# Kernel tuning notes

Measured on AMD Instinct MI355X. Metric: run time of the kernel, lower is better.

## Reference

```python
import jax, jax.numpy as jnp
import numpy as np

B, N, D = 8, 2048, 512
H, DH = 8, 64
SCALE = DH ** -0.5


def setup_inputs() -> dict:
    key = jax.random.key(0)
    ks = jax.random.split(key, 7)
    x = jax.random.normal(ks[0], (B, N, D), dtype=jnp.float32)
    mask = jax.random.uniform(ks[1], (B, N, N), dtype=jnp.float32)
    Wq = jax.random.normal(ks[2], (D, H * DH), dtype=jnp.float32) * (D ** -0.5)
    Wk = jax.random.normal(ks[3], (D, H * DH), dtype=jnp.float32) * (D ** -0.5)
    Wv = jax.random.normal(ks[4], (D, H * DH), dtype=jnp.float32) * (D ** -0.5)
    Wo = jax.random.normal(ks[5], (H * DH, D), dtype=jnp.float32) * ((H * DH) ** -0.5)
    bo = jnp.zeros((D,), dtype=jnp.float32)
    return {"x": x, "mask": mask, "Wq": Wq, "Wk": Wk, "Wv": Wv, "Wo": Wo, "bo": bo}


def reference(x, mask, Wq, Wk, Wv, Wo, bo):
    b, n, d = x.shape
    # QKV projections -> [b, h, n, dh]
    q = (x @ Wq).reshape(b, n, H, DH).transpose(0, 2, 1, 3)
    k = (x @ Wk).reshape(b, n, H, DH).transpose(0, 2, 1, 3)
    v = (x @ Wv).reshape(b, n, H, DH).transpose(0, 2, 1, 3)
    # scores with multiplicative structural mask bias: dots * (1 + M)
    dots = jnp.einsum('bhid,bhjd->bhij', q, k) * SCALE
    dots = dots * (1.0 + mask[:, None, :, :])
    attn = jax.nn.softmax(dots, axis=-1)  # dropout is identity in eval
    out = jnp.einsum('bhij,bhjd->bhid', attn, v)
    out = out.transpose(0, 2, 1, 3).reshape(b, n, H * DH)
    return out @ Wo + bo
```

## Files before the change

### kernel.cpp

```cpp
#include <hip/hip_runtime.h>

typedef __bf16 bf16;
typedef __bf16 bf16x8 __attribute__((ext_vector_type(8)));
typedef float  f32x4  __attribute__((ext_vector_type(4)));

#define B_  8
#define N_  2048
#define D_  512
#define H_  8
#define DH_ 64
static constexpr float SC2 = 0.18033688011112042f;

#if defined(__has_builtin)
#if __has_builtin(__builtin_amdgcn_exp2f)
#define EXP2(x) __builtin_amdgcn_exp2f(x)
#else
#define EXP2(x) exp2f(x)
#endif
#else
#define EXP2(x) exp2f(x)
#endif

__device__ __forceinline__ f32x4 mfma16(bf16x8 a, bf16x8 b, f32x4 c) {
  return __builtin_amdgcn_mfma_f32_16x16x32_bf16(a, b, c, 0, 0, 0);
}

__device__ __forceinline__ void gload_lds16(const void* g, void* l) {
  __builtin_amdgcn_global_load_lds((__attribute__((address_space(1))) void*)g,
                                   (__attribute__((address_space(3))) void*)l, 16, 0, 0);
}

__global__ void k_cvt_x(const float* __restrict__ x, bf16* __restrict__ xb) {
  int i = blockIdx.x * blockDim.x + threadIdx.x;
  const float4* p = (const float4*)x;
  float4 a = p[2*i], b = p[2*i+1];
  bf16x8 o;
  o[0]=(bf16)a.x; o[1]=(bf16)a.y; o[2]=(bf16)a.z; o[3]=(bf16)a.w;
  o[4]=(bf16)b.x; o[5]=(bf16)b.y; o[6]=(bf16)b.z; o[7]=(bf16)b.w;
  ((bf16x8*)xb)[i] = o;
}

__global__ void k_wt(const float* __restrict__ w, bf16* __restrict__ wt) {
  __shared__ float t[64][65];
  const int c0 = blockIdx.x * 64, k0 = blockIdx.y * 64;
  const int r = threadIdx.x >> 2, q4 = (threadIdx.x & 3) * 16;
#pragma unroll
  for (int j = 0; j < 16; j += 4) {
    float4 v = *(const float4*)(w + (k0 + r) * 512 + c0 + q4 + j);
    t[r][q4+j] = v.x; t[r][q4+j+1] = v.y; t[r][q4+j+2] = v.z; t[r][q4+j+3] = v.w;
  }
  __syncthreads();
  const int c = threadIdx.x >> 2, kq = (threadIdx.x & 3) * 16;
  bf16x8 o0, o1;
#pragma unroll
  for (int j = 0; j < 8; ++j) { o0[j] = (bf16)t[kq+j][c]; o1[j] = (bf16)t[kq+8+j][c]; }
  *(bf16x8*)(wt + (c0 + c) * 512 + k0 + kq) = o0;
  *(bf16x8*)(wt + (c0 + c) * 512 + k0 + kq + 8) = o1;
}

template<int MODE>
__global__ void k_gemm(const bf16* __restrict__ A, const bf16* __restrict__ Bt,
                       bf16* __restrict__ qo, bf16* __restrict__ ko, bf16* __restrict__ vo,
                       float* __restrict__ outp, const float* __restrict__ bo) {
  __shared__ bf16 lA[128 * 64];
  __shared__ bf16 lB[128 * 64];
  const int tid = threadIdx.x;
  const int wid = tid >> 6, lane = tid & 63;
  const int l15 = lane & 15, lq = lane >> 4;
  const int wr = wid >> 1, wc = wid & 1;
  const long long rowtile = (long long)blockIdx.x * 128;
  const long long coltile = (long long)blockIdx.y * 128;

  const bf16* gA[4]; const bf16* gB[4];
  bf16* lAc[4]; bf16* lBc[4];
#pragma unroll
  for (int i = 0; i < 4; ++i) {
    int ci = wid * 4 + i;
    int row = ci * 8 + (lane >> 3);
    int c8 = (lane & 7) ^ (row & 7);
    gA[i] = A + (rowtile + row) * 512 + c8 * 8;
    gB[i] = Bt + (coltile + row) * 512 + c8 * 8;
    lAc[i] = &lA[ci * 512];
    lBc[i] = &lB[ci * 512];
  }
  unsigned aoff[4][2], boff[4][2];
#pragma unroll
  for (int mi = 0; mi < 4; ++mi) {
#pragma unroll
    for (int ks = 0; ks < 2; ++ks) {
      int R = l15 + 16 * mi + 64 * wr;
      aoff[mi][ks] = R * 128 + ((((ks << 2) | lq) ^ (R & 7)) << 4);
      int Rb = l15 + 16 * mi + 64 * wc;
      boff[mi][ks] = Rb * 128 + ((((ks << 2) | lq) ^ (Rb & 7)) << 4);
    }
  }
  f32x4 acc[4][4] = {};
  for (int kt = 0; kt < 8; ++kt) {
#pragma unroll
    for (int i = 0; i < 4; ++i) gload_lds16(gA[i], lAc[i]);
#pragma unroll
    for (int i = 0; i < 4; ++i) gload_lds16(gB[i], lBc[i]);
#pragma unroll
    for (int i = 0; i < 4; ++i) { gA[i] += 64; gB[i] += 64; }
    __syncthreads();
#pragma unroll
    for (int ks = 0; ks < 2; ++ks) {
      bf16x8 af[4], bfr[4];
#pragma unroll
      for (int mi = 0; mi < 4; ++mi) af[mi] = *(const bf16x8*)((const char*)lA + aoff[mi][ks]);
#pragma unroll
      for (int nf = 0; nf < 4; ++nf) bfr[nf] = *(const bf16x8*)((const char*)lB + boff[nf][ks]);
#pragma unroll
      for (int mi = 0; mi < 4; ++mi)
#pragma unroll
        for (int nf = 0; nf < 4; ++nf)
          acc[mi][nf] = mfma16(af[mi], bfr[nf], acc[mi][nf]);
    }
    __syncthreads();
  }
  if (MODE == 0) {
#pragma unroll
    for (int nf = 0; nf < 4; ++nf) {
      const int col = (int)coltile + 64 * wc + nf * 16 + l15;
      const int mat = col >> 9, c5 = col & 511, hh = c5 >> 6, dh = c5 & 63;
#pragma unroll
      for (int mi = 0; mi < 4; ++mi) {
#pragma unroll
        for (int r = 0; r < 4; ++r) {
          const int R = (int)rowtile + 64 * wr + mi * 16 + lq * 4 + r;
          const int bb = R >> 11, n = R & 2047;
          const bf16 bv = (bf16)acc[mi][nf][r];
          const long long bh = bb * 8 + hh;
          if (mat == 0)      qo[(bh * 2048 + n) * 64 + dh] = bv;
          else if (mat == 1) ko[(bh * 2048 + n) * 64 + dh] = bv;
          else               vo[(bh * 64 + dh) * 2048 + n] = bv;
        }
      }
    }
  } else {
#pragma unroll
    for (int nf = 0; nf < 4; ++nf) {
      const int col = (int)coltile + 64 * wc + nf * 16 + l15;
      const float bias = bo[col];
#pragma unroll
      for (int mi = 0; mi < 4; ++mi)
#pragma unroll
        for (int r = 0; r < 4; ++r) {
          const long long R = rowtile + 64 * wr + mi * 16 + lq * 4 + r;
          outp[R * 512 + col] = acc[mi][nf][r] + bias;
        }
    }
  }
}

__global__ __launch_bounds__(512, 4) void k_attn(
    const bf16* __restrict__ qb, const bf16* __restrict__ kb, const bf16* __restrict__ vt,
    const float* __restrict__ mask, bf16* __restrict__ ao) {
  __shared__ bf16 kvb[2][2][64 * 64];
  __shared__ bf16 pb[8][16 * 64];
  const int tid = threadIdx.x;
  const int wid = tid >> 6, lane = tid & 63;
  const int l15 = lane & 15, lq = lane >> 4;
  const int p = blockIdx.x;
  const int xcd = p & 7, kk = p >> 3;
  const int g = xcd * 16 + (kk >> 3), h = kk & 7;
  const int b = g >> 4, qt = g & 15;
  const long long bh = b * 8 + h;
  const bf16* Q = qb + bh * (2048ll * 64);
  const bf16* K = kb + bh * (2048ll * 64);
  const bf16* V = vt + bh * (64ll * 2048);
  const int qrow0 = qt * 128 + wid * 16;
  const float* mbase = mask + ((long long)b * 2048 + qrow0 + lq * 4) * 2048 + l15;

  const int srow = tid >> 3;
  const int sc = (tid & 7) ^ (srow & 7);
  const bf16* kg = K + srow * 64 + sc * 8;
  const bf16* vg = V + srow * 2048 + sc * 8;
  bf16* kl0 = &kvb[0][0][tid * 8]; bf16* vl0 = &kvb[0][1][tid * 8];
  bf16* kl1 = &kvb[1][0][tid * 8]; bf16* vl1 = &kvb[1][1][tid * 8];
  char* pw = (char*)&pb[wid][0];

  bf16x8 qf[2];
#pragma unroll
  for (int ks = 0; ks < 2; ++ks)
    qf[ks] = *(const bf16x8*)(Q + (qrow0 + l15) * 64 + ks * 32 + lq * 8);

  f32x4 o[4] = {};
  float lsum[4] = {};
  float mA[16], mB[16];

  auto mload = [&](float (&m)[16], int jb) {
#pragma unroll
    for (int nf = 0; nf < 4; ++nf)
#pragma unroll
      for (int r = 0; r < 4; ++r)
        m[nf * 4 + r] = mbase[r * 2048 + jb + nf * 16];
  };

  auto compute = [&](int bi, const float (&m)[16]) {
    const bf16* kbL = &kvb[bi][0][0];
    const bf16* vbL = &kvb[bi][1][0];
    f32x4 s[4];
#pragma unroll
    for (int nf = 0; nf < 4; ++nf) {
      const int row = nf * 16 + l15;
      const bf16x8 kf = *(const bf16x8*)(kbL + row * 64 + ((lq ^ (row & 7)) << 3));
      f32x4 z = {0.f, 0.f, 0.f, 0.f};
      s[nf] = mfma16(qf[0], kf, z);
    }
#pragma unroll
    for (int nf = 0; nf < 4; ++nf) {
      const int row = nf * 16 + l15;
      const bf16x8 kf = *(const bf16x8*)(kbL + row * 64 + (((4 + lq) ^ (row & 7)) << 3));
      s[nf] = mfma16(qf[1], kf, s[nf]);
    }
#pragma unroll
    for (int nf = 0; nf < 4; ++nf) {
#pragma unroll
      for (int r = 0; r < 4; ++r) {
        const float dsc = s[nf][r] * SC2;
        const float pe = EXP2(fmaf(dsc, m[nf * 4 + r], dsc));
        lsum[r] += pe;
        const int colL = nf * 16 + l15;
        const int slot = ((colL >> 3) ^ (lq << 1) ^ r) & 7;
        *(bf16*)(pw + (lq * 4 + r) * 128 + slot * 16 + ((colL & 7) << 1)) = (bf16)pe;
      }
    }
#pragma unroll
    for (int ks = 0; ks < 2; ++ks) {
      const int c = ks * 4 + lq;
      const int slotp = (c ^ ((l15 >> 2) << 1) ^ (l15 & 3)) & 7;
      const bf16x8 pa = *(const bf16x8*)(pw + l15 * 128 + slotp * 16);
#pragma unroll
      for (int nf = 0; nf < 4; ++nf) {
        const int row = nf * 16 + l15;
        const bf16x8 vf = *(const bf16x8*)(vbL + row * 64 + ((c ^ (row & 7)) << 3));
        o[nf] = mfma16(pa, vf, o[nf]);
      }
    }
  };

  gload_lds16(kg, kl0); gload_lds16(vg, vl0);
  mload(mA, 0);
  __syncthreads();

  for (int jt = 0; jt < 32; jt += 2) {
    gload_lds16(kg + (jt + 1) * 4096, kl1);
    gload_lds16(vg + (jt + 1) * 64, vl1);
    mload(mB, (jt + 1) * 64);
    compute(0, mA);
    __syncthreads();
    if (jt + 2 < 32) {
      gload_lds16(kg + (jt + 2) * 4096, kl0);
      gload_lds16(vg + (jt + 2) * 64, vl0);
      mload(mA, (jt + 2) * 64);
    }
    compute(1, mB);
    __syncthreads();
  }

  float rinv[4];
#pragma unroll
  for (int r = 0; r < 4; ++r) {
    float v2 = lsum[r];
    v2 += __shfl_xor(v2, 1); v2 += __shfl_xor(v2, 2);
    v2 += __shfl_xor(v2, 4); v2 += __shfl_xor(v2, 8);
    rinv[r] = 1.0f / v2;
  }
#pragma unroll
  for (int nf = 0; nf < 4; ++nf)
#pragma unroll
    for (int r = 0; r < 4; ++r) {
      const long long rowg = (long long)b * 2048 + qrow0 + lq * 4 + r;
      ao[rowg * 512 + h * 64 + nf * 16 + l15] = (bf16)(o[nf][r] * rinv[r]);
    }
}

extern "C" void kernel_launch(void* const* d_in, const int* in_sizes, int n_in,
                              void* d_out, int out_size, void* d_ws, size_t ws_size,
                              hipStream_t stream) {
  const float* x    = (const float*)d_in[0];
  const float* mask = (const float*)d_in[1];
  const float* Wq   = (const float*)d_in[2];
  const float* Wk   = (const float*)d_in[3];
  const float* Wv   = (const float*)d_in[4];
  const float* Wo   = (const float*)d_in[5];
  const float* bo   = (const float*)d_in[6];
  float* out = (float*)d_out;
  char* ws = (char*)d_ws;

  const size_t SZ_XB = (size_t)16384 * 512 * 2;
  const size_t SZ_W3 = (size_t)1536 * 512 * 2;
  const size_t SZ_WO = (size_t)512 * 512 * 2;
  const size_t SZ_T  = (size_t)64 * 2048 * 64 * 2;

  bf16* xb    = (bf16*)ws;
  bf16* wqkvT = (bf16*)(ws + SZ_XB);
  bf16* woT   = (bf16*)(ws + SZ_XB + SZ_W3);
  bf16* qbuf  = (bf16*)(ws + SZ_XB + SZ_W3 + SZ_WO);
  bf16* kbuf  = (bf16*)((char*)qbuf + SZ_T);
  bf16* vtb   = (bf16*)((char*)kbuf + SZ_T);
  bf16* aob   = xb;

  k_cvt_x<<<dim3(4096), dim3(256), 0, stream>>>(x, xb);
  k_wt<<<dim3(8, 8), dim3(256), 0, stream>>>(Wq, wqkvT);
  k_wt<<<dim3(8, 8), dim3(256), 0, stream>>>(Wk, wqkvT + 512 * 512);
  k_wt<<<dim3(8, 8), dim3(256), 0, stream>>>(Wv, wqkvT + 2 * 512 * 512);
  k_wt<<<dim3(8, 8), dim3(256), 0, stream>>>(Wo, woT);
  k_gemm<0><<<dim3(128, 12), dim3(256), 0, stream>>>(xb, wqkvT, qbuf, kbuf, vtb, nullptr, nullptr);
  k_attn<<<dim3(1024), dim3(512), 0, stream>>>(qbuf, kbuf, vtb, mask, aob);
  k_gemm<1><<<dim3(128, 4), dim3(256), 0, stream>>>(aob, woT, nullptr, nullptr, nullptr, out, bo);
}
```

Baseline: 227.3 us.

## Keep softmax probabilities in registers via transposed QK MFMA and permlane swaps

The attention kernel now computes S^T (K as the A operand) so each lane holds four consecutive key columns for one query row. P goes straight from registers into the PV MFMA operand through permlane32/16 swaps instead of a round trip through LDS. V fragments are read directly from global/L2 rather than staged in LDS, and mask loads become 16-byte nontemporal vector loads. Blocks shrink to 256 threads with 64 query rows each and the grid grows to 2048, which trades more redundant K/V traffic for less LDS pressure and more blocks in flight.

```diff
diff --git a/kernel.cpp b/kernel.cpp
--- a/kernel.cpp
+++ b/kernel.cpp
@@ -3,6 +3,7 @@
 typedef __bf16 bf16;
 typedef __bf16 bf16x8 __attribute__((ext_vector_type(8)));
 typedef float  f32x4  __attribute__((ext_vector_type(4)));
+typedef unsigned u32x4 __attribute__((ext_vector_type(4)));
 
 #define B_  8
 #define N_  2048
@@ -21,6 +22,12 @@
 #define EXP2(x) exp2f(x)
 #endif
 
+#if defined(__has_builtin)
+#if __has_builtin(__builtin_amdgcn_permlane32_swap) && __has_builtin(__builtin_amdgcn_permlane16_swap)
+#define HAVE_PLSWAP 1
+#endif
+#endif
+
 __device__ __forceinline__ f32x4 mfma16(bf16x8 a, bf16x8 b, f32x4 c) {
   return __builtin_amdgcn_mfma_f32_16x16x32_bf16(a, b, c, 0, 0, 0);
 }
@@ -28,6 +35,12 @@
 __device__ __forceinline__ void gload_lds16(const void* g, void* l) {
   __builtin_amdgcn_global_load_lds((__attribute__((address_space(1))) void*)g,
                                    (__attribute__((address_space(3))) void*)l, 16, 0, 0);
+}
+
+__device__ __forceinline__ unsigned cvt_pk_bf16(float lo, float hi) {
+  unsigned r;
+  asm("v_cvt_pk_bf16_f32 %0, %1, %2" : "=v"(r) : "v"(lo), "v"(hi));
+  return r;
 }
 
 __global__ void k_cvt_x(const float* __restrict__ x, bf16* __restrict__ xb) {
@@ -153,32 +166,33 @@
   }
 }
 
-__global__ __launch_bounds__(512, 4) void k_attn(
+__global__ __launch_bounds__(256, 4) void k_attn(
     const bf16* __restrict__ qb, const bf16* __restrict__ kb, const bf16* __restrict__ vt,
     const float* __restrict__ mask, bf16* __restrict__ ao) {
-  __shared__ bf16 kvb[2][2][64 * 64];
-  __shared__ bf16 pb[8][16 * 64];
+  __shared__ __align__(16) bf16 kls[2][64 * 64];
   const int tid = threadIdx.x;
   const int wid = tid >> 6, lane = tid & 63;
   const int l15 = lane & 15, lq = lane >> 4;
   const int p = blockIdx.x;
-  const int xcd = p & 7, kk = p >> 3;
-  const int g = xcd * 16 + (kk >> 3), h = kk & 7;
-  const int b = g >> 4, qt = g & 15;
+  const int xcd = p & 7, rr = p >> 3;
+  const int g = xcd * 32 + (rr >> 3), h = rr & 7;
+  const int b = g >> 5, qt = g & 31;
   const long long bh = b * 8 + h;
   const bf16* Q = qb + bh * (2048ll * 64);
   const bf16* K = kb + bh * (2048ll * 64);
   const bf16* V = vt + bh * (64ll * 2048);
-  const int qrow0 = qt * 128 + wid * 16;
-  const float* mbase = mask + ((long long)b * 2048 + qrow0 + lq * 4) * 2048 + l15;
-
-  const int srow = tid >> 3;
-  const int sc = (tid & 7) ^ (srow & 7);
-  const bf16* kg = K + srow * 64 + sc * 8;
-  const bf16* vg = V + srow * 2048 + sc * 8;
-  bf16* kl0 = &kvb[0][0][tid * 8]; bf16* vl0 = &kvb[0][1][tid * 8];
-  bf16* kl1 = &kvb[1][0][tid * 8]; bf16* vl1 = &kvb[1][1][tid * 8];
-  char* pw = (char*)&pb[wid][0];
+  const int qrow0 = qt * 64 + wid * 16;
+  const float* mptr = mask + ((long long)b * 2048 + qrow0 + l15) * 2048 + lq * 4;
+  const bf16* Vr[4];
+#pragma unroll
+  for (int nf = 0; nf < 4; ++nf) Vr[nf] = V + (nf * 16 + l15) * 2048 + lq * 8;
+
+  const int sr0 = tid >> 3, sr1 = sr0 + 32;
+  const int sc0 = (tid & 7) ^ (sr0 & 7), sc1 = (tid & 7) ^ (sr1 & 7);
+  const bf16* kg0 = K + sr0 * 64 + sc0 * 8;
+  const bf16* kg1 = K + sr1 * 64 + sc1 * 8;
+  bf16* kd0[2] = { &kls[0][tid * 8], &kls[1][tid * 8] };
+  bf16* kd1[2] = { &kls[0][2048 + tid * 8], &kls[1][2048 + tid * 8] };
 
   bf16x8 qf[2];
 #pragma unroll
@@ -186,93 +200,120 @@
     qf[ks] = *(const bf16x8*)(Q + (qrow0 + l15) * 64 + ks * 32 + lq * 8);
 
   f32x4 o[4] = {};
-  float lsum[4] = {};
-  float mA[16], mB[16];
-
-  auto mload = [&](float (&m)[16], int jb) {
+  float lsum = 0.f;
+  f32x4 mA[4], mB[4];
+
+  auto stageK = [&](int buf, int jt) {
+    gload_lds16(kg0 + jt * 4096, kd0[buf]);
+    gload_lds16(kg1 + jt * 4096, kd1[buf]);
+  };
+  auto mload = [&](f32x4 (&m)[4], int jb) {
 #pragma unroll
     for (int nf = 0; nf < 4; ++nf)
-#pragma unroll
-      for (int r = 0; r < 4; ++r)
-        m[nf * 4 + r] = mbase[r * 2048 + jb + nf * 16];
+      m[nf] = __builtin_nontemporal_load((const f32x4*)(mptr + jb + nf * 16));
   };
 
-  auto compute = [&](int bi, const float (&m)[16]) {
-    const bf16* kbL = &kvb[bi][0][0];
-    const bf16* vbL = &kvb[bi][1][0];
+  auto compute = [&](const bf16* kbL, const f32x4 (&m)[4], int jb) {
+    bf16x8 vf0[4], vf1[4];
+#pragma unroll
+    for (int nf = 0; nf < 4; ++nf) {
+      vf0[nf] = *(const bf16x8*)(Vr[nf] + jb);
+      vf1[nf] = *(const bf16x8*)(Vr[nf] + jb + 32);
+    }
     f32x4 s[4];
 #pragma unroll
     for (int nf = 0; nf < 4; ++nf) {
       const int row = nf * 16 + l15;
       const bf16x8 kf = *(const bf16x8*)(kbL + row * 64 + ((lq ^ (row & 7)) << 3));
       f32x4 z = {0.f, 0.f, 0.f, 0.f};
-      s[nf] = mfma16(qf[0], kf, z);
+      s[nf] = mfma16(kf, qf[0], z);
     }
 #pragma unroll
     for (int nf = 0; nf < 4; ++nf) {
       const int row = nf * 16 + l15;
       const bf16x8 kf = *(const bf16x8*)(kbL + row * 64 + (((4 + lq) ^ (row & 7)) << 3));
-      s[nf] = mfma16(qf[1], kf, s[nf]);
-    }
-#pragma unroll
-    for (int nf = 0; nf < 4; ++nf) {
-#pragma unroll
-      for (int r = 0; r < 4; ++r) {
-        const float dsc = s[nf][r] * SC2;
-        const float pe = EXP2(fmaf(dsc, m[nf * 4 + r], dsc));
-        lsum[r] += pe;
-        const int colL = nf * 16 + l15;
-        const int slot = ((colL >> 3) ^ (lq << 1) ^ r) & 7;
-        *(bf16*)(pw + (lq * 4 + r) * 128 + slot * 16 + ((colL & 7) << 1)) = (bf16)pe;
+      s[nf] = mfma16(kf, qf[1], s[nf]);
+    }
+    unsigned w[4][2];
+#pragma unroll
+    for (int nf = 0; nf < 4; ++nf) {
+      float mp0 = fmaf(m[nf][0], SC2, SC2);
+      float mp1 = fmaf(m[nf][1], SC2, SC2);
+      float mp2 = fmaf(m[nf][2], SC2, SC2);
+      float mp3 = fmaf(m[nf][3], SC2, SC2);
+      float pe0 = EXP2(s[nf][0] * mp0);
+      float pe1 = EXP2(s[nf][1] * mp1);
+      float pe2 = EXP2(s[nf][2] * mp2);
+      float pe3 = EXP2(s[nf][3] * mp3);
+      lsum += ((pe0 + pe1) + (pe2 + pe3));
+      w[nf][0] = cvt_pk_bf16(pe0, pe1);
+      w[nf][1] = cvt_pk_bf16(pe2, pe3);
+    }
+    unsigned pa0[4], pa1[4];
+#ifdef HAVE_PLSWAP
+#pragma unroll
+    for (int t = 0; t < 2; ++t) {
+      auto sA = __builtin_amdgcn_permlane32_swap(w[0][t], w[1][t], false, false);
+      auto sB = __builtin_amdgcn_permlane16_swap(sA[0], sA[1], false, false);
+      pa0[t] = sB[0]; pa0[t + 2] = sB[1];
+      auto sC = __builtin_amdgcn_permlane32_swap(w[2][t], w[3][t], false, false);
+      auto sD = __builtin_amdgcn_permlane16_swap(sC[0], sC[1], false, false);
+      pa1[t] = sD[0]; pa1[t + 2] = sD[1];
+    }
+#else
+    {
+      const int basel = l15 + ((lq & 1) << 5);
+#pragma unroll
+      for (int t = 0; t < 2; ++t) {
+        int sel0 = (lq & 2) ? (int)w[1][t] : (int)w[0][t];
+        int sel1 = (lq & 2) ? (int)w[3][t] : (int)w[2][t];
+        pa0[t]     = (unsigned)__shfl(sel0, basel);
+        pa0[t + 2] = (unsigned)__shfl(sel0, basel + 16);
+        pa1[t]     = (unsigned)__shfl(sel1, basel);
+        pa1[t + 2] = (unsigned)__shfl(sel1, basel + 16);
       }
     }
-#pragma unroll
-    for (int ks = 0; ks < 2; ++ks) {
-      const int c = ks * 4 + lq;
-      const int slotp = (c ^ ((l15 >> 2) << 1) ^ (l15 & 3)) & 7;
-      const bf16x8 pa = *(const bf16x8*)(pw + l15 * 128 + slotp * 16);
-#pragma unroll
-      for (int nf = 0; nf < 4; ++nf) {
-        const int row = nf * 16 + l15;
-        const bf16x8 vf = *(const bf16x8*)(vbL + row * 64 + ((c ^ (row & 7)) << 3));
-        o[nf] = mfma16(pa, vf, o[nf]);
-      }
-    }
+#endif
+    u32x4 ua = {pa0[0], pa0[1], pa0[2], pa0[3]};
+    u32x4 ub = {pa1[0], pa1[1], pa1[2], pa1[3]};
+    const bf16x8 paA = __builtin_bit_cast(bf16x8, ua);
+    const bf16x8 paB = __builtin_bit_cast(bf16x8, ub);
+#pragma unroll
+    for (int nf = 0; nf < 4; ++nf) o[nf] = mfma16(paA, vf0[nf], o[nf]);
+#pragma unroll
+    for (int nf = 0; nf < 4; ++nf) o[nf] = mfma16(paB, vf1[nf], o[nf]);
   };
 
-  gload_lds16(kg, kl0); gload_lds16(vg, vl0);
+  stageK(0, 0);
   mload(mA, 0);
   __syncthreads();
 
   for (int jt = 0; jt < 32; jt += 2) {
-    gload_lds16(kg + (jt + 1) * 4096, kl1);
-    gload_lds16(vg + (jt + 1) * 64, vl1);
+    stageK(1, jt + 1);
     mload(mB, (jt + 1) * 64);
-    compute(0, mA);
+    compute(&kls[0][0], mA, jt * 64);
     __syncthreads();
     if (jt + 2 < 32) {
-      gload_lds16(kg + (jt + 2) * 4096, kl0);
-      gload_lds16(vg + (jt + 2) * 64, vl0);
+      stageK(0, jt + 2);
       mload(mA, (jt + 2) * 64);
     }
-    compute(1, mB);
+    compute(&kls[1][0], mB, (jt + 1) * 64);
     __syncthreads();
   }
 
-  float rinv[4];
-#pragma unroll
-  for (int r = 0; r < 4; ++r) {
-    float v2 = lsum[r];
-    v2 += __shfl_xor(v2, 1); v2 += __shfl_xor(v2, 2);
-    v2 += __shfl_xor(v2, 4); v2 += __shfl_xor(v2, 8);
-    rinv[r] = 1.0f / v2;
-  }
+  lsum += __shfl_xor(lsum, 16);
+  lsum += __shfl_xor(lsum, 32);
+  const float rinv = 1.0f / lsum;
+  float rv[4];
+#pragma unroll
+  for (int r = 0; r < 4; ++r)
+    rv[r] = __shfl(rinv, ((lane & 48) >> 2) + r);
 #pragma unroll
   for (int nf = 0; nf < 4; ++nf)
 #pragma unroll
     for (int r = 0; r < 4; ++r) {
       const long long rowg = (long long)b * 2048 + qrow0 + lq * 4 + r;
-      ao[rowg * 512 + h * 64 + nf * 16 + l15] = (bf16)(o[nf][r] * rinv[r]);
+      ao[rowg * 512 + h * 64 + nf * 16 + l15] = (bf16)(o[nf][r] * rv[r]);
     }
 }
 
@@ -308,6 +349,6 @@
   k_wt<<<dim3(8, 8), dim3(256), 0, stream>>>(Wv, wqkvT + 2 * 512 * 512);
   k_wt<<<dim3(8, 8), dim3(256), 0, stream>>>(Wo, woT);
   k_gemm<0><<<dim3(128, 12), dim3(256), 0, stream>>>(xb, wqkvT, qbuf, kbuf, vtb, nullptr, nullptr);
-  k_attn<<<dim3(1024), dim3(512), 0, stream>>>(qbuf, kbuf, vtb, mask, aob);
+  k_attn<<<dim3(2048), dim3(256), 0, stream>>>(qbuf, kbuf, vtb, mask, aob);
   k_gemm<1><<<dim3(128, 4), dim3(256), 0, stream>>>(aob, woT, nullptr, nullptr, nullptr, out, bo);
 }
```

Result: slower. 484.1 us (+113.0%).
